# Performance work log

Measured on AMD Instinct MI355X. Metric: run time of the kernel, lower is better.

Reference implementation:

```python
import jax, jax.numpy as jnp
import numpy as np

OUT_FEATURES = 11008  # LLaMA-7B FFN intermediate
IN_FEATURES = 4096    # d_model
N_TOKENS = 16         # small M -> weight-traffic bound
SCALE = 0.01
ZERO_POINT = 0


def setup_inputs() -> dict:
    key = jax.random.key(0)
    k1, k2 = jax.random.split(key)
    x = jax.random.normal(k1, (N_TOKENS, IN_FEATURES), dtype=jnp.float32)
    weight_int8 = jax.random.randint(
        k2, (OUT_FEATURES, IN_FEATURES), -128, 128, dtype=jnp.int32
    ).astype(jnp.int8)
    return {
        "x": x,
        "weight_int8": weight_int8,
        "scale": SCALE,
        "zero_point": ZERO_POINT,
    }


def reference(x, weight_int8, scale, zero_point):
    # Dequantize INT8 weight to fp32 (same elementwise pass as the torch module)
    weight_fp = (weight_int8.astype(jnp.float32) - zero_point) * scale  # [out, in]
    # F.linear(x, W) == x @ W.T
    return jnp.einsum("ti,oi->to", x, weight_fp)
```

## Files before the change

### kernel.cpp

```cpp
#include <hip/hip_runtime.h>
#include <hip/hip_bf16.h>
#include <stdint.h>


#define M_TOK 16
#define K_DIM 4096
#define N_OUT 11008

typedef int v4i __attribute__((ext_vector_type(4)));

__global__ __launch_bounds__(256) void quant_x_kernel(
    const float* __restrict__ x, int8_t* __restrict__ xh,
    int8_t* __restrict__ xl, float* __restrict__ s1_out,
    float* __restrict__ sumx_out) {
  const int t = blockIdx.x;
  const int tid = threadIdx.x;
  const float4* xv = (const float4*)(x + (long)t * K_DIM) + tid * 4;

  float vals[16];
  float m = 0.0f, s = 0.0f;
#pragma unroll
  for (int j = 0; j < 4; ++j) {
    float4 f = xv[j];
    vals[j * 4 + 0] = f.x; vals[j * 4 + 1] = f.y;
    vals[j * 4 + 2] = f.z; vals[j * 4 + 3] = f.w;
    m = fmaxf(m, fmaxf(fmaxf(fabsf(f.x), fabsf(f.y)),
                       fmaxf(fabsf(f.z), fabsf(f.w))));
    s += f.x + f.y + f.z + f.w;
  }
#pragma unroll
  for (int off = 32; off > 0; off >>= 1) {
    m = fmaxf(m, __shfl_xor(m, off));
    s += __shfl_xor(s, off);
  }
  __shared__ float lm[4], ls[4];
  const int w = tid >> 6;
  if ((tid & 63) == 0) { lm[w] = m; ls[w] = s; }
  __syncthreads();
  m = fmaxf(fmaxf(lm[0], lm[1]), fmaxf(lm[2], lm[3]));
  s = ls[0] + ls[1] + ls[2] + ls[3];

  const float s1 = (m > 0.0f) ? (m * (1.0f / 127.0f)) : 1.0f;
  const float inv = 1.0f / s1;
  if (tid == 0) { s1_out[t] = s1; sumx_out[t] = s; }

  int hq[16], lq[16];
#pragma unroll
  for (int j = 0; j < 16; ++j) {
    float xf = vals[j];
    float h = rintf(xf * inv);
    h = fminf(fmaxf(h, -127.0f), 127.0f);
    float resid = xf - h * s1;
    float l = rintf(resid * inv * 256.0f);
    l = fminf(fmaxf(l, -128.0f), 127.0f);
    hq[j] = (int)h;
    lq[j] = (int)l;
  }
  int4 hv, lv;
  int* hp = (int*)&hv;
  int* lp = (int*)&lv;
#pragma unroll
  for (int d = 0; d < 4; ++d) {
    uint32_t hw = 0, lw = 0;
#pragma unroll
    for (int j = 0; j < 4; ++j) {
      hw |= (uint32_t)(hq[d * 4 + j] & 0xff) << (8 * j);
      lw |= (uint32_t)(lq[d * 4 + j] & 0xff) << (8 * j);
    }
    hp[d] = (int)hw;
    lp[d] = (int)lw;
  }
  ((int4*)xh)[(long)t * 256 + tid] = hv;
  ((int4*)xl)[(long)t * 256 + tid] = lv;
}

__global__ __launch_bounds__(256) void qgemm_kernel(
    const int* __restrict__ W, const int8_t* __restrict__ xh,
    const int8_t* __restrict__ xl, const float* __restrict__ s1,
    const float* __restrict__ sumx, const float* __restrict__ scale_p,
    const int* __restrict__ zp_p, float* __restrict__ out) {
  const int tid = threadIdx.x;
  const int lane = tid & 63;
  const int w = tid >> 6;
  const int obase = blockIdx.x * 16;
  const int n = lane & 15;
  const int g = lane >> 4;
  const int r0 = w * 4;

  __shared__ v4i wbuf[2][256];
  __shared__ float red[4][16 * 17];

  const v4i* Wr0 = (const v4i*)(W + (long)(obase + r0 + 0) * K_DIM) + lane;
  const v4i* Wr1 = (const v4i*)(W + (long)(obase + r0 + 1) * K_DIM) + lane;
  const v4i* Wr2 = (const v4i*)(W + (long)(obase + r0 + 2) * K_DIM) + lane;
  const v4i* Wr3 = (const v4i*)(W + (long)(obase + r0 + 3) * K_DIM) + lane;

  int wr_idx[4];
#pragma unroll
  for (int r = 0; r < 4; ++r) {
    const int row = r0 + r;
    wr_idx[r] = row * 64 + (lane ^ ((row & 7) << 2));
  }
  const int rd_idx = n * 16 + ((4 * w + g) ^ (n & 7));

  const v4i* Ah = (const v4i*)xh + (n * 256 + w * 4 + g);
  const v4i* Al = (const v4i*)xl + (n * 256 + w * 4 + g);

  v4i wreg[2][4];
  wreg[0][0] = Wr0[0];
  wreg[0][1] = Wr1[0];
  wreg[0][2] = Wr2[0];
  wreg[0][3] = Wr3[0];

  v4i accH = {0, 0, 0, 0};
  v4i accL = {0, 0, 0, 0};

#pragma unroll
  for (int c = 0; c < 16; ++c) {
    const int cur = c & 1;
    if (c + 1 < 16) {
      const int nxt = (c + 1) & 1;
      wreg[nxt][0] = Wr0[(c + 1) * 64];
      wreg[nxt][1] = Wr1[(c + 1) * 64];
      wreg[nxt][2] = Wr2[(c + 1) * 64];
      wreg[nxt][3] = Wr3[(c + 1) * 64];
    }
    uint32_t* wb = (uint32_t*)wbuf[cur];
#pragma unroll
    for (int r = 0; r < 4; ++r) {
      v4i q = wreg[cur][r];
      uint32_t packed = ((uint32_t)q.x & 0xffu) |
                        (((uint32_t)q.y & 0xffu) << 8) |
                        (((uint32_t)q.z & 0xffu) << 16) |
                        (((uint32_t)q.w & 0xffu) << 24);
      wb[wr_idx[r]] = packed;
    }
    __syncthreads();
    const v4i b = wbuf[cur][rd_idx];
    accH = __builtin_amdgcn_mfma_i32_16x16x64_i8(Ah[c * 16], b, accH, 0, 0, 0);
    accL = __builtin_amdgcn_mfma_i32_16x16x64_i8(Al[c * 16], b, accL, 0, 0, 0);
  }

#pragma unroll
  for (int r = 0; r < 4; ++r) {
    float f = (float)accH[r] + (float)accL[r] * (1.0f / 256.0f);
    const int t = g * 4 + r;
    red[w][t * 17 + n] = f;
  }
  __syncthreads();

  const int t = tid >> 4;
  const int col = tid & 15;
  const float sum = red[0][t * 17 + col] + red[1][t * 17 + col] +
                    red[2][t * 17 + col] + red[3][t * 17 + col];
  const float sc = scale_p[0];
  const float zp = (float)zp_p[0];
  const float o = sc * (s1[t] * sum) - sc * zp * sumx[t];
  out[(long)t * N_OUT + obase + col] = o;
}

extern "C" void kernel_launch(void* const* d_in, const int* in_sizes, int n_in,
                              void* d_out, int out_size, void* d_ws,
                              size_t ws_size, hipStream_t stream) {
  const float* x = (const float*)d_in[0];
  const int* Wq = (const int*)d_in[1];
  const float* scale_p = (const float*)d_in[2];
  const int* zp_p = (const int*)d_in[3];
  float* out = (float*)d_out;

  int8_t* xh = (int8_t*)d_ws;
  int8_t* xl = xh + (long)M_TOK * K_DIM;
  float* s1 = (float*)(xl + (long)M_TOK * K_DIM);
  float* sumx = s1 + M_TOK;

  quant_x_kernel<<<M_TOK, 256, 0, stream>>>(x, xh, xl, s1, sumx);
  qgemm_kernel<<<N_OUT / 16, 256, 0, stream>>>(Wq, xh, xl, s1, sumx, scale_p,
                                               zp_p, out);
}
```

Measured before the change: 254.0 us.

## Deepen weight prefetch to two chunks and replace syncthreads with LDS-only barrier

The K loop now issues global weight loads two chunks ahead and packs the next chunk into the alternate LDS buffer while the MFMAs consume the current one. The per-iteration __syncthreads is replaced by an lgkmcnt(0) wait plus s_barrier, so the barrier no longer waits on in-flight global loads. Activation fragment loads are also hoisted to the top of each iteration. The aim is to keep more weight traffic in flight in this latency-bound GEMV-like kernel. The cost is extra register pressure and correctness that depends on the hand-placed wait counts.

```diff
diff --git a/kernel.cpp b/kernel.cpp
--- a/kernel.cpp
+++ b/kernel.cpp
@@ -111,34 +111,56 @@
   wreg[0][1] = Wr1[0];
   wreg[0][2] = Wr2[0];
   wreg[0][3] = Wr3[0];
-
-  v4i accH = {0, 0, 0, 0};
-  v4i accL = {0, 0, 0, 0};
-
-#pragma unroll
-  for (int c = 0; c < 16; ++c) {
-    const int cur = c & 1;
-    if (c + 1 < 16) {
-      const int nxt = (c + 1) & 1;
-      wreg[nxt][0] = Wr0[(c + 1) * 64];
-      wreg[nxt][1] = Wr1[(c + 1) * 64];
-      wreg[nxt][2] = Wr2[(c + 1) * 64];
-      wreg[nxt][3] = Wr3[(c + 1) * 64];
-    }
-    uint32_t* wb = (uint32_t*)wbuf[cur];
+  wreg[1][0] = Wr0[64];
+  wreg[1][1] = Wr1[64];
+  wreg[1][2] = Wr2[64];
+  wreg[1][3] = Wr3[64];
+  {
+    uint32_t* wb = (uint32_t*)wbuf[0];
 #pragma unroll
     for (int r = 0; r < 4; ++r) {
-      v4i q = wreg[cur][r];
+      v4i q = wreg[0][r];
       uint32_t packed = ((uint32_t)q.x & 0xffu) |
                         (((uint32_t)q.y & 0xffu) << 8) |
                         (((uint32_t)q.z & 0xffu) << 16) |
                         (((uint32_t)q.w & 0xffu) << 24);
       wb[wr_idx[r]] = packed;
     }
-    __syncthreads();
+  }
+  asm volatile("s_waitcnt lgkmcnt(0)" ::: "memory");
+  __builtin_amdgcn_s_barrier();
+
+  v4i accH = {0, 0, 0, 0};
+  v4i accL = {0, 0, 0, 0};
+
+#pragma unroll
+  for (int c = 0; c < 16; ++c) {
+    const int cur = c & 1;
+    v4i ah = Ah[c * 16];
+    v4i al = Al[c * 16];
+    if (c + 2 < 16) {
+      wreg[cur][0] = Wr0[(c + 2) * 64];
+      wreg[cur][1] = Wr1[(c + 2) * 64];
+      wreg[cur][2] = Wr2[(c + 2) * 64];
+      wreg[cur][3] = Wr3[(c + 2) * 64];
+    }
+    if (c + 1 < 16) {
+      uint32_t* wb = (uint32_t*)wbuf[cur ^ 1];
+#pragma unroll
+      for (int r = 0; r < 4; ++r) {
+        v4i q = wreg[cur ^ 1][r];
+        uint32_t packed = ((uint32_t)q.x & 0xffu) |
+                          (((uint32_t)q.y & 0xffu) << 8) |
+                          (((uint32_t)q.z & 0xffu) << 16) |
+                          (((uint32_t)q.w & 0xffu) << 24);
+        wb[wr_idx[r]] = packed;
+      }
+    }
     const v4i b = wbuf[cur][rd_idx];
-    accH = __builtin_amdgcn_mfma_i32_16x16x64_i8(Ah[c * 16], b, accH, 0, 0, 0);
-    accL = __builtin_amdgcn_mfma_i32_16x16x64_i8(Al[c * 16], b, accL, 0, 0, 0);
+    accH = __builtin_amdgcn_mfma_i32_16x16x64_i8(ah, b, accH, 0, 0, 0);
+    accL = __builtin_amdgcn_mfma_i32_16x16x64_i8(al, b, accL, 0, 0, 0);
+    asm volatile("s_waitcnt lgkmcnt(0)" ::: "memory");
+    __builtin_amdgcn_s_barrier();
   }
 
 #pragma unroll
```

Measured after the change: 254.2 us. No clear change (+0.1%).

## Stage four K-chunks per barrier with larger LDS double buffer in qgemm

Applied to the files above, without the earlier changes.

Each qgemm stage now loads four 1024-element K chunks of weights per row instead of one, storing them into a larger swizzled LDS buffer. The main loop drops from 16 barrier-separated steps to 4, each issuing four MFMA pairs. Each wave now covers a contiguous quarter of every stage's K range, where before the four waves took interleaved slices. The aim is fewer barriers and more global loads in flight per thread, which helps a weight-bandwidth-bound GEMV. The cost is more registers (16 v4i staged loads) and much more LDS per block (32KB), which can reduce occupancy.

```diff
diff --git a/kernel.cpp b/kernel.cpp
--- a/kernel.cpp
+++ b/kernel.cpp
@@ -87,7 +87,7 @@
   const int g = lane >> 4;
   const int r0 = w * 4;
 
-  __shared__ v4i wbuf[2][256];
+  __shared__ uint32_t wbuf[2][16 * 256];
   __shared__ float red[4][16 * 17];
 
   const v4i* Wr0 = (const v4i*)(W + (long)(obase + r0 + 0) * K_DIM) + lane;
@@ -95,50 +95,66 @@
   const v4i* Wr2 = (const v4i*)(W + (long)(obase + r0 + 2) * K_DIM) + lane;
   const v4i* Wr3 = (const v4i*)(W + (long)(obase + r0 + 3) * K_DIM) + lane;
 
-  int wr_idx[4];
+  int wbase[4];
 #pragma unroll
   for (int r = 0; r < 4; ++r) {
     const int row = r0 + r;
-    wr_idx[r] = row * 64 + (lane ^ ((row & 7) << 2));
+    wbase[r] = row * 256 + ((((lane >> 2) ^ (row & 7)) << 2) | (lane & 3));
   }
-  const int rd_idx = n * 16 + ((4 * w + g) ^ (n & 7));
 
-  const v4i* Ah = (const v4i*)xh + (n * 256 + w * 4 + g);
-  const v4i* Al = (const v4i*)xl + (n * 256 + w * 4 + g);
+  const v4i* Ah = (const v4i*)xh + n * 256 + w * 16 + g;
+  const v4i* Al = (const v4i*)xl + n * 256 + w * 16 + g;
 
-  v4i wreg[2][4];
-  wreg[0][0] = Wr0[0];
-  wreg[0][1] = Wr1[0];
-  wreg[0][2] = Wr2[0];
-  wreg[0][3] = Wr3[0];
+  v4i wr_[4][4];
+#define STAGE_LOAD(c)                                                        \
+  {                                                                          \
+    _Pragma("unroll") for (int i = 0; i < 4; ++i) {                          \
+      wr_[i][0] = Wr0[(c) * 256 + i * 64];                                   \
+      wr_[i][1] = Wr1[(c) * 256 + i * 64];                                   \
+      wr_[i][2] = Wr2[(c) * 256 + i * 64];                                   \
+      wr_[i][3] = Wr3[(c) * 256 + i * 64];                                   \
+    }                                                                        \
+  }
+#define STAGE_WRITE(buf)                                                     \
+  {                                                                          \
+    uint32_t* wb = wbuf[buf];                                                \
+    _Pragma("unroll") for (int i = 0; i < 4; ++i) {                          \
+      _Pragma("unroll") for (int r = 0; r < 4; ++r) {                        \
+        v4i q = wr_[i][r];                                                   \
+        uint32_t p = ((uint32_t)q.x & 0xffu) |                               \
+                     (((uint32_t)q.y & 0xffu) << 8) |                        \
+                     (((uint32_t)q.z & 0xffu) << 16) |                       \
+                     (((uint32_t)q.w & 0xffu) << 24);                        \
+        wb[wbase[r] + i * 64] = p;                                           \
+      }                                                                      \
+    }                                                                        \
+  }
+
+  STAGE_LOAD(0);
+  STAGE_WRITE(0);
+  asm volatile("s_waitcnt lgkmcnt(0)" ::: "memory");
+  __builtin_amdgcn_s_barrier();
 
   v4i accH = {0, 0, 0, 0};
   v4i accL = {0, 0, 0, 0};
 
 #pragma unroll
-  for (int c = 0; c < 16; ++c) {
+  for (int c = 0; c < 4; ++c) {
     const int cur = c & 1;
-    if (c + 1 < 16) {
-      const int nxt = (c + 1) & 1;
-      wreg[nxt][0] = Wr0[(c + 1) * 64];
-      wreg[nxt][1] = Wr1[(c + 1) * 64];
-      wreg[nxt][2] = Wr2[(c + 1) * 64];
-      wreg[nxt][3] = Wr3[(c + 1) * 64];
+    if (c + 1 < 4) STAGE_LOAD(c + 1);
+#pragma unroll
+    for (int it = 0; it < 4; ++it) {
+      const int j = w * 16 + it * 4 + g;
+      const v4i b =
+          *(const v4i*)&wbuf[cur][n * 256 + ((j ^ (n & 7)) << 2)];
+      accH = __builtin_amdgcn_mfma_i32_16x16x64_i8(Ah[c * 64 + it * 4], b,
+                                                   accH, 0, 0, 0);
+      accL = __builtin_amdgcn_mfma_i32_16x16x64_i8(Al[c * 64 + it * 4], b,
+                                                   accL, 0, 0, 0);
     }
-    uint32_t* wb = (uint32_t*)wbuf[cur];
-#pragma unroll
-    for (int r = 0; r < 4; ++r) {
-      v4i q = wreg[cur][r];
-      uint32_t packed = ((uint32_t)q.x & 0xffu) |
-                        (((uint32_t)q.y & 0xffu) << 8) |
-                        (((uint32_t)q.z & 0xffu) << 16) |
-                        (((uint32_t)q.w & 0xffu) << 24);
-      wb[wr_idx[r]] = packed;
-    }
-    __syncthreads();
-    const v4i b = wbuf[cur][rd_idx];
-    accH = __builtin_amdgcn_mfma_i32_16x16x64_i8(Ah[c * 16], b, accH, 0, 0, 0);
-    accL = __builtin_amdgcn_mfma_i32_16x16x64_i8(Al[c * 16], b, accL, 0, 0, 0);
+    if (c + 1 < 4) STAGE_WRITE(cur ^ 1);
+    asm volatile("s_waitcnt lgkmcnt(0)" ::: "memory");
+    __builtin_amdgcn_s_barrier();
   }
 
 #pragma unroll
```

After: 254.1 us, median of 2. Within noise of the previous version (+0.0%).
